# Optimization experiments

Hardware: AMD Instinct MI355X
Metric: run time of the kernel (lower is better)

The kernel has to match this reference:

```python
import jax, jax.numpy as jnp
import numpy as np

INF = 1000000000000.0
B, H, EMB = 64, 512, 512
V = 32000
S_ENC, S_SEQ = 512, 512
ENC2 = 512  # 2 * encoder_hidden_dim
NUM_OOV = 50


def setup_inputs() -> dict:
    key = jax.random.key(0)
    ks = jax.random.split(key, 24)
    s = 0.02
    nrm = lambda k, shp: jax.random.normal(k, shp, jnp.float32) * s
    inp = {}
    inp["input_ids"] = jax.random.randint(ks[0], (B,), 0, V)
    inp["prev_context"] = jax.random.normal(ks[1], (B, H), jnp.float32)
    inp["h0"] = jax.random.normal(ks[2], (1, B, H), jnp.float32)
    inp["c0"] = jax.random.normal(ks[3], (1, B, H), jnp.float32)
    inp["encoder_outputs"] = jax.random.normal(ks[4], (B, S_ENC, H), jnp.float32)
    inp["seqs_encoding"] = jax.random.normal(ks[5], (B, S_SEQ, ENC2), jnp.float32)
    inp["seqs_encoding_mask"] = jax.random.randint(ks[6], (B, S_SEQ), 0, 2).astype(bool)
    ext = jax.random.randint(ks[7], (B, S_SEQ), 0, V + NUM_OOV)
    inp["ext_idx"] = ext.at[0, 0].set(V + NUM_OOV - 1)  # pin max so num_oov=NUM_OOV
    # parameters (torch Linear convention: y = x @ W.T + b)
    inp["embed"] = nrm(ks[8], (V, EMB))
    inp["W_reduce"] = nrm(ks[9], (EMB, EMB + H)); inp["b_reduce"] = jnp.zeros((EMB,), jnp.float32)
    inp["W_key"] = nrm(ks[10], (H, H)); inp["b_key"] = jnp.zeros((H,), jnp.float32)
    inp["W_comb"] = nrm(ks[11], (H, 2 * H)); inp["b_comb"] = jnp.zeros((H,), jnp.float32)
    inp["W_seqkey"] = nrm(ks[12], (H, ENC2))
    inp["W_ih"] = nrm(ks[13], (4 * H, EMB)); inp["W_hh"] = nrm(ks[14], (4 * H, H))
    inp["b_ih"] = jnp.zeros((4 * H,), jnp.float32); inp["b_hh"] = jnp.zeros((4 * H,), jnp.float32)
    inp["W_out"] = nrm(ks[15], (V, H)); inp["b_out"] = jnp.zeros((V,), jnp.float32)
    return inp


def reference(input_ids, prev_context, h0, c0, encoder_outputs, seqs_encoding,
              seqs_encoding_mask, ext_idx, embed, W_reduce, b_reduce, W_key, b_key,
              W_comb, b_comb, W_seqkey, W_ih, W_hh, b_ih, b_hh, W_out, b_out):
    # embed + (dropout is identity at p=0 / eval) + reduce
    embedded = embed[input_ids]                                   # [B, EMB]
    x = jnp.concatenate([embedded, prev_context], axis=1) @ W_reduce.T + b_reduce  # [B, EMB]
    # single-step, single-layer LSTM (PyTorch gate order i, f, g, o)
    h, c = h0[0], c0[0]
    gates = x @ W_ih.T + b_ih + h @ W_hh.T + b_hh                 # [B, 4H]
    i, f, g, o = jnp.split(gates, 4, axis=-1)
    c1 = jax.nn.sigmoid(f) * c + jax.nn.sigmoid(i) * jnp.tanh(g)
    h1 = jax.nn.sigmoid(o) * jnp.tanh(c1)                         # [B, H]
    output = h1
    # masked attention over encoder_outputs
    enc_mask = encoder_outputs.sum(axis=-1) == 0                  # [B, S_enc]
    keys = encoder_outputs @ W_key.T + b_key                      # [B, S_enc, H]
    energies = jnp.einsum('bsh,bh->bs', keys, output)
    energies = jnp.where(enc_mask, 1e-12, energies)
    attn_weights = jax.nn.softmax(energies, axis=-1)
    context = jnp.einsum('bs,bsh->bh', attn_weights, encoder_outputs)  # [B, H]
    combined = jnp.tanh(jnp.concatenate([output, context], axis=1) @ W_comb.T + b_comb)
    logits = combined @ W_out.T + b_out                           # [B, V]
    # masked attention energies over token sequence for the copy mechanism
    seq_keys = jnp.tanh(seqs_encoding @ W_seqkey.T)               # [B, S_seq, H]
    seq_energies = jnp.einsum('bsh,bh->bs', seq_keys, output)
    seq_energies = jnp.where(seqs_encoding_mask, 1e-12, seq_energies)
    # extended vocab + scatter_max pointer-copy
    extended = jnp.concatenate([logits, jnp.zeros((B, NUM_OOV), logits.dtype)], axis=1)  # [B, V+OOV]
    copy = jnp.full_like(extended, -INF)
    copy = copy.at[jnp.arange(B)[:, None], ext_idx].max(seq_energies)
    copy = jnp.where(copy == -INF, 0.0, copy)
    out = extended + copy
    out = jnp.where(out == 0.0, -INF, out)
    out = jax.nn.log_softmax(out, axis=1)
    return (out, context, h1[None], c1[None], attn_weights)
```

## Files before the change

### kernel.cpp

```cpp
#include <hip/hip_runtime.h>
#include <math.h>

#define B_N    64
#define H_N    512
#define V_N    32000
#define S_N    512
#define VEXT   32050
#define INF_F  1000000000000.0f

typedef __attribute__((ext_vector_type(4))) float floatx4;
typedef __attribute__((ext_vector_type(8))) __bf16 bf16x8;

#define OFF_OUT0 0
#define OFF_CTX  (B_N * VEXT)
#define OFF_H1   (OFF_CTX + B_N * H_N)
#define OFF_C1   (OFF_H1 + B_N * H_N)
#define OFF_ATTN (OFF_C1 + B_N * H_N)

#define WS_FLAG   0
#define WS_X      16
#define WS_GATES  (WS_X + B_N * H_N)
#define WS_Q      (WS_GATES + B_N * 4 * H_N)
#define WS_KB     (WS_Q + B_N * H_N)
#define WS_EN     (WS_KB + B_N)
#define WS_COMB   (WS_EN + B_N * S_N)
#define WS_SEQE   (WS_COMB + B_N * H_N)
#define WS_WSKBF  (WS_SEQE + B_N * S_N)
#define WS_LOGITS (WS_WSKBF + (H_N * H_N) / 2)
#define WS_COPY   (WS_LOGITS + B_N * V_N)
#define WS_RMAX   (WS_COPY + B_N * VEXT)
#define WS_RSUM   (WS_RMAX + B_N)

__device__ __forceinline__ float sigm(float x) { return 1.0f / (1.0f + expf(-x)); }

__device__ __forceinline__ unsigned short f2bf(float f) {
    unsigned u = __float_as_uint(f);
    u += 0x7fffu + ((u >> 16) & 1u);
    return (unsigned short)(u >> 16);
}
__device__ __forceinline__ float bf2f(unsigned short h) {
    return __uint_as_float(((unsigned)h) << 16);
}

__device__ __forceinline__ unsigned enc_f(float f) {
    unsigned u = __float_as_uint(f);
    return (u & 0x80000000u) ? ~u : (u | 0x80000000u);
}
__device__ __forceinline__ float dec_f(unsigned e) {
    unsigned u = (e & 0x80000000u) ? (e & 0x7fffffffu) : ~e;
    return __uint_as_float(u);
}

__global__ __launch_bounds__(256) void kPre(
        const unsigned int* __restrict__ m, int* __restrict__ flag,
        const float* __restrict__ W, unsigned short* __restrict__ swzh,
        unsigned short* __restrict__ swzl, unsigned int* __restrict__ copyenc,
        unsigned int* __restrict__ rmax, float* __restrict__ rsum,
        float* __restrict__ ctx) {
    const int bx = blockIdx.x, tid = threadIdx.x;
    if (bx == 0) {
        __shared__ int any;
        if (tid == 0) any = 0;
        __syncthreads();
        int loc = 0;
        for (int i = tid; i < 8192; i += 256) loc |= (m[i] > 1u) ? 1 : 0;
        if (loc) any = 1;
        __syncthreads();
        if (tid == 0) *flag = any;
    } else if (bx < 129) {
        const int g = (bx - 1) * 256 + tid;
        const int t = g >> 10, kc = (g >> 6) & 15, lane = g & 63;
        const int r = t * 16 + (lane & 15);
        const int k = kc * 32 + (lane >> 4) * 8;
        const float* src = W + (size_t)r * 512 + k;
        ushort4 h0, h1, l0, l1;
        const float4 v0 = *(const float4*)(src);
        const float4 v1 = *(const float4*)(src + 4);
        h0.x = f2bf(v0.x); l0.x = f2bf(v0.x - bf2f(h0.x));
        h0.y = f2bf(v0.y); l0.y = f2bf(v0.y - bf2f(h0.y));
        h0.z = f2bf(v0.z); l0.z = f2bf(v0.z - bf2f(h0.z));
        h0.w = f2bf(v0.w); l0.w = f2bf(v0.w - bf2f(h0.w));
        h1.x = f2bf(v1.x); l1.x = f2bf(v1.x - bf2f(h1.x));
        h1.y = f2bf(v1.y); l1.y = f2bf(v1.y - bf2f(h1.y));
        h1.z = f2bf(v1.z); l1.z = f2bf(v1.z - bf2f(h1.z));
        h1.w = f2bf(v1.w); l1.w = f2bf(v1.w - bf2f(h1.w));
        *(ushort4*)(swzh + (size_t)g * 8) = h0;
        *(ushort4*)(swzh + (size_t)g * 8 + 4) = h1;
        *(ushort4*)(swzl + (size_t)g * 8) = l0;
        *(ushort4*)(swzl + (size_t)g * 8 + 4) = l1;
    } else if (bx < 2133) {
        const int fb = bx - 129;
        const unsigned NE = enc_f(-INF_F);
        if (fb == 0 && tid < B_N) {
            rmax[tid] = 0u;
            rsum[tid] = 0.0f;
        }
        int i0 = (fb * 256 + tid) * 4;
#pragma unroll
        for (int k = 0; k < 4; k++) {
            int i = i0 + k;
            if (i < B_N * VEXT) copyenc[i] = NE;
        }
    } else {
        const int zb = bx - 2133;
        const float4 z4 = {0.f, 0.f, 0.f, 0.f};
        *(float4*)(ctx + (size_t)(zb * 256 + tid) * 4) = z4;
    }
}

__global__ __launch_bounds__(256) void kEmbedReduce(
        const int* __restrict__ ids, const float* __restrict__ embed,
        const float* __restrict__ pctx, const float* __restrict__ Wred,
        const float* __restrict__ bred, float* __restrict__ x) {
    __shared__ float xc[1024];
    const int tid = threadIdx.x;
    const int b = blockIdx.x >> 1, half = blockIdx.x & 1;
    const float* er = embed + (size_t)ids[b] * 512;
    xc[tid] = er[tid];               xc[tid + 256] = er[tid + 256];
    xc[512 + tid] = pctx[b * 512 + tid]; xc[512 + tid + 256] = pctx[b * 512 + tid + 256];
    __syncthreads();
    const int j = half * 256 + tid;
    const float4* w4 = (const float4*)(Wred + (size_t)j * 1024);
    const float4* x4 = (const float4*)xc;
    float acc = bred[j];
    for (int k = 0; k < 256; k++) {
        float4 w = w4[k], xv = x4[k];
        acc += w.x * xv.x + w.y * xv.y + w.z * xv.z + w.w * xv.w;
    }
    x[b * 512 + j] = acc;
}

__global__ __launch_bounds__(256) void kGates(
        const float* __restrict__ x, const float* __restrict__ h0,
        const float* __restrict__ Wih, const float* __restrict__ Whh,
        const float* __restrict__ bih, const float* __restrict__ bhh,
        float* __restrict__ gates) {
    __shared__ float xl[512], hl[512];
    const int tid = threadIdx.x;
    const int b = blockIdx.x >> 3, part = blockIdx.x & 7;
    xl[tid] = x[b * 512 + tid];  xl[tid + 256] = x[b * 512 + tid + 256];
    hl[tid] = h0[b * 512 + tid]; hl[tid + 256] = h0[b * 512 + tid + 256];
    __syncthreads();
    const int j = part * 256 + tid;
    const float4* wi4 = (const float4*)(Wih + (size_t)j * 512);
    const float4* wh4 = (const float4*)(Whh + (size_t)j * 512);
    const float4* x4 = (const float4*)xl;
    const float4* h4 = (const float4*)hl;
    float acc = bih[j] + bhh[j];
    for (int k = 0; k < 128; k++) {
        float4 w = wi4[k], xv = x4[k];
        acc += w.x * xv.x + w.y * xv.y + w.z * xv.z + w.w * xv.w;
    }
    for (int k = 0; k < 128; k++) {
        float4 w = wh4[k], hv = h4[k];
        acc += w.x * hv.x + w.y * hv.y + w.z * hv.z + w.w * hv.w;
    }
    gates[(size_t)b * 2048 + j] = acc;
}

__global__ __launch_bounds__(256) void kLstm(
        const float* __restrict__ gates, const float* __restrict__ c0,
        float* __restrict__ h1o, float* __restrict__ c1o) {
    const int idx = blockIdx.x * 256 + threadIdx.x;
    const int b = idx >> 9, j = idx & 511;
    const float gi = gates[(size_t)b * 2048 + j];
    const float gf = gates[(size_t)b * 2048 + 512 + j];
    const float gg = gates[(size_t)b * 2048 + 1024 + j];
    const float go = gates[(size_t)b * 2048 + 1536 + j];
    const float cp = c0[idx];
    const float c1 = sigm(gf) * cp + sigm(gi) * tanhf(gg);
    const float h1 = sigm(go) * tanhf(c1);
    h1o[idx] = h1;
    c1o[idx] = c1;
}

__global__ __launch_bounds__(256) void kQ(
        const float* __restrict__ h1, const float* __restrict__ Wkey,
        const float* __restrict__ bkey, float* __restrict__ q, float* __restrict__ kb) {
    __shared__ float hl[512];
    __shared__ float rd[256];
    const int tid = threadIdx.x;
    const int b = blockIdx.x >> 1, half = blockIdx.x & 1;
    hl[tid] = h1[b * 512 + tid]; hl[tid + 256] = h1[b * 512 + tid + 256];
    __syncthreads();
    const int k = half * 256 + tid;
    float acc = 0.f;
#pragma unroll 4
    for (int h = 0; h < 512; h++) acc += hl[h] * Wkey[(size_t)h * 512 + k];
    q[b * 512 + k] = acc;
    if (half == 0) {
        float p = bkey[tid] * hl[tid] + bkey[tid + 256] * hl[tid + 256];
        rd[tid] = p; __syncthreads();
        for (int st = 128; st > 0; st >>= 1) {
            if (tid < st) rd[tid] += rd[tid + st];
            __syncthreads();
        }
        if (tid == 0) kb[b] = rd[0];
    }
}

__global__ __launch_bounds__(256) void kEnergies(
        const float* __restrict__ enc, const float* __restrict__ q,
        const float* __restrict__ kb, float* __restrict__ energ) {
    __shared__ float ql[512];
    __shared__ float pe[256], ps[256];
    const int tid = threadIdx.x;
    const int b = blockIdx.x >> 2;
    const int sc = (blockIdx.x & 3) * 128;
    ql[tid] = q[b * 512 + tid]; ql[tid + 256] = q[b * 512 + tid + 256];
    __syncthreads();
    const int r = tid & 127, hi = tid >> 7;
    const float4* row4 = (const float4*)(enc + (size_t)(b * 512 + sc + r) * 512 + hi * 256);
    const float4* q4 = (const float4*)(ql + hi * 256);
    float e = 0.f, ssum = 0.f;
#pragma unroll 4
    for (int k = 0; k < 64; k++) {
        float4 ev = row4[k], qv = q4[k];
        e += ev.x * qv.x + ev.y * qv.y + ev.z * qv.z + ev.w * qv.w;
        ssum += ev.x + ev.y + ev.z + ev.w;
    }
    pe[tid] = e; ps[tid] = ssum;
    __syncthreads();
    if (tid < 128) {
        float ee = pe[tid] + pe[tid + 128] + kb[b];
        float sm = ps[tid] + ps[tid + 128];
        if (sm == 0.0f) ee = 1e-12f;
        energ[b * 512 + sc + tid] = ee;
    }
}

__global__ __launch_bounds__(256) void kSoftmax(
        const float* __restrict__ energ, float* __restrict__ attn) {
    __shared__ float el[512];
    __shared__ float rd[256];
    const int tid = threadIdx.x, b = blockIdx.x;
    el[tid] = energ[b * 512 + tid]; el[tid + 256] = energ[b * 512 + tid + 256];
    __syncthreads();
    rd[tid] = fmaxf(el[tid], el[tid + 256]); __syncthreads();
    for (int st = 128; st > 0; st >>= 1) {
        if (tid < st) rd[tid] = fmaxf(rd[tid], rd[tid + st]);
        __syncthreads();
    }
    const float m = rd[0]; __syncthreads();
    float v0 = expf(el[tid] - m), v1 = expf(el[tid + 256] - m);
    rd[tid] = v0 + v1; __syncthreads();
    for (int st = 128; st > 0; st >>= 1) {
        if (tid < st) rd[tid] += rd[tid + st];
        __syncthreads();
    }
    const float inv = 1.0f / rd[0];
    attn[b * 512 + tid] = v0 * inv;
    attn[b * 512 + tid + 256] = v1 * inv;
}

__global__ __launch_bounds__(256) void kContext(
        const float* __restrict__ enc, const float* __restrict__ attn,
        float* __restrict__ ctx) {
    __shared__ float al[64];
    const int tid = threadIdx.x;
    const int b = blockIdx.x >> 3, sc = (blockIdx.x & 7) * 64;
    if (tid < 64) al[tid] = attn[b * 512 + sc + tid];
    __syncthreads();
    float a0 = 0.f, a1 = 0.f;
    for (int s = 0; s < 64; s++) {
        const float* row = enc + (size_t)(b * 512 + sc + s) * 512;
        const float av = al[s];
        a0 += av * row[tid];
        a1 += av * row[tid + 256];
    }
    atomicAdd(&ctx[b * 512 + tid], a0);
    atomicAdd(&ctx[b * 512 + tid + 256], a1);
}

__global__ __launch_bounds__(256) void kCombined(
        const float* __restrict__ h1, const float* __restrict__ ctx,
        const float* __restrict__ Wcomb, const float* __restrict__ bcomb,
        float* __restrict__ comb) {
    __shared__ float hc[1024];
    const int tid = threadIdx.x;
    const int b = blockIdx.x >> 1, half = blockIdx.x & 1;
    hc[tid] = h1[b * 512 + tid];        hc[tid + 256] = h1[b * 512 + tid + 256];
    hc[512 + tid] = ctx[b * 512 + tid]; hc[512 + tid + 256] = ctx[b * 512 + tid + 256];
    __syncthreads();
    const int j = half * 256 + tid;
    const float4* w4 = (const float4*)(Wcomb + (size_t)j * 1024);
    const float4* x4 = (const float4*)hc;
    float acc = bcomb[j];
    for (int k = 0; k < 256; k++) {
        float4 w = w4[k], xv = x4[k];
        acc += w.x * xv.x + w.y * xv.y + w.z * xv.z + w.w * xv.w;
    }
    comb[b * 512 + j] = tanhf(acc);
}

__global__ __launch_bounds__(256) void kLogits(
        const float* __restrict__ comb, const float* __restrict__ Wout,
        const float* __restrict__ bout, float* __restrict__ logits) {
    __shared__ float cl[4][32][64];
    const int tid = threadIdx.x;
    const int vt = tid & 63, kq = tid >> 6;
    const int v = blockIdx.x * 64 + vt;
    float acc[64];
#pragma unroll
    for (int i = 0; i < 64; i++) acc[i] = 0.f;
    for (int kc = 0; kc < 4; kc++) {
        __syncthreads();
        {
            const float4* s4 = (const float4*)(comb + (size_t)vt * 512 + kq * 128 + kc * 32);
#pragma unroll
            for (int qq = 0; qq < 8; qq++) {
                float4 vv = s4[qq];
                cl[kq][qq * 4 + 0][vt] = vv.x; cl[kq][qq * 4 + 1][vt] = vv.y;
                cl[kq][qq * 4 + 2][vt] = vv.z; cl[kq][qq * 4 + 3][vt] = vv.w;
            }
        }
        __syncthreads();
        float wreg[32];
        const float4* w4 = (const float4*)(Wout + (size_t)v * 512 + kq * 128 + kc * 32);
#pragma unroll
        for (int qq = 0; qq < 8; qq++) {
            float4 wv = w4[qq];
            wreg[qq * 4 + 0] = wv.x; wreg[qq * 4 + 1] = wv.y;
            wreg[qq * 4 + 2] = wv.z; wreg[qq * 4 + 3] = wv.w;
        }
#pragma unroll
        for (int kk = 0; kk < 32; kk++) {
            const float wv = wreg[kk];
            const float4* cp = (const float4*)&cl[kq][kk][0];
#pragma unroll
            for (int b4 = 0; b4 < 16; b4++) {
                float4 c4 = cp[b4];
                acc[b4 * 4 + 0] += wv * c4.x; acc[b4 * 4 + 1] += wv * c4.y;
                acc[b4 * 4 + 2] += wv * c4.z; acc[b4 * 4 + 3] += wv * c4.w;
            }
        }
    }
    float* red = &cl[0][0][0];
    __syncthreads();
    if (kq >= 2) {
#pragma unroll
        for (int b = 0; b < 64; b++) red[(kq - 2) * 4096 + vt * 64 + b] = acc[b];
    }
    __syncthreads();
    if (kq < 2) {
#pragma unroll
        for (int b = 0; b < 64; b++) acc[b] += red[kq * 4096 + vt * 64 + b];
    }
    __syncthreads();
    if (kq == 1) {
#pragma unroll
        for (int b = 0; b < 64; b++) red[vt * 64 + b] = acc[b];
    }
    __syncthreads();
    if (kq == 0) {
        const float bo = bout[v];
#pragma unroll
        for (int b = 0; b < 64; b++)
            logits[(size_t)b * 32000 + v] = acc[b] + red[vt * 64 + b] + bo;
    }
}

#define ACH 136
__global__ __launch_bounds__(512, 2) void kSeqGemm(
        const float* __restrict__ seqs, const unsigned short* __restrict__ swzh,
        const unsigned short* __restrict__ swzl, const float* __restrict__ h1g,
        const void* __restrict__ mask, const int* __restrict__ extix,
        const int* __restrict__ flag, unsigned int* __restrict__ copyenc) {
    __shared__ unsigned short a_hi[128 * ACH];
    __shared__ unsigned short a_lo[128 * ACH];
    __shared__ float h1l[512];
    __shared__ float partf[8][128];
    const int tid = threadIdx.x;
    const int m0 = blockIdx.x * 128;
    const int b = blockIdx.x >> 2;
    const int w = tid >> 6;
    const int lane = tid & 63;
    const int quad = lane >> 4;
    const int c16 = lane & 15;

    h1l[tid] = h1g[b * 512 + tid];

    floatx4 acc[8][4];
    const floatx4 zf = {0.f, 0.f, 0.f, 0.f};
#pragma unroll
    for (int i = 0; i < 8; i++)
#pragma unroll
        for (int j = 0; j < 4; j++) acc[i][j] = zf;

    const size_t boff = (size_t)(w * 64) * 512 + (size_t)lane * 8;
    const unsigned short* bh = swzh + boff;
    const unsigned short* bl = swzl + boff;

    const int srow = tid >> 2, sq = tid & 3;

    for (int c = 0; c < 4; c++) {
        __syncthreads();
        {
            const float* src = seqs + (size_t)(m0 + srow) * 512 + c * 128 + sq * 32;
            unsigned short* dh = &a_hi[srow * ACH + sq * 32];
            unsigned short* dl = &a_lo[srow * ACH + sq * 32];
#pragma unroll
            for (int i = 0; i < 8; i++) {
                float4 v = *(const float4*)(src + i * 4);
                ushort4 hv, lv;
                hv.x = f2bf(v.x); lv.x = f2bf(v.x - bf2f(hv.x));
                hv.y = f2bf(v.y); lv.y = f2bf(v.y - bf2f(hv.y));
                hv.z = f2bf(v.z); lv.z = f2bf(v.z - bf2f(hv.z));
                hv.w = f2bf(v.w); lv.w = f2bf(v.w - bf2f(hv.w));
                *(ushort4*)(dh + i * 4) = hv;
                *(ushort4*)(dl + i * 4) = lv;
            }
        }
        __syncthreads();
#pragma unroll
        for (int kcl = 0; kcl < 4; kcl++) {
            const int kc = c * 4 + kcl;
            bf16x8 bhf[4], blf[4];
#pragma unroll
            for (int nt = 0; nt < 4; nt++) {
                bhf[nt] = *(const bf16x8*)(bh + (size_t)(nt * 16 + kc) * 512);
                blf[nt] = *(const bf16x8*)(bl + (size_t)(nt * 16 + kc) * 512);
            }
#pragma unroll
            for (int ms = 0; ms < 8; ms++) {
                bf16x8 ah = *(const bf16x8*)&a_hi[(ms * 16 + c16) * ACH + kcl * 32 + quad * 8];
                bf16x8 al = *(const bf16x8*)&a_lo[(ms * 16 + c16) * ACH + kcl * 32 + quad * 8];
#pragma unroll
                for (int nt = 0; nt < 4; nt++) {
                    acc[ms][nt] = __builtin_amdgcn_mfma_f32_16x16x32_bf16(
                        ah, bhf[nt], acc[ms][nt], 0, 0, 0);
                    acc[ms][nt] = __builtin_amdgcn_mfma_f32_16x16x32_bf16(
                        al, bhf[nt], acc[ms][nt], 0, 0, 0);
                    acc[ms][nt] = __builtin_amdgcn_mfma_f32_16x16x32_bf16(
                        ah, blf[nt], acc[ms][nt], 0, 0, 0);
                }
            }
        }
    }

    float psum[32];
#pragma unroll
    for (int i = 0; i < 32; i++) psum[i] = 0.f;
#pragma unroll
    for (int ms = 0; ms < 8; ms++)
#pragma unroll
        for (int nt = 0; nt < 4; nt++) {
            const float hv = h1l[w * 64 + nt * 16 + c16];
#pragma unroll
            for (int r = 0; r < 4; r++)
                psum[ms * 4 + r] += tanhf(acc[ms][nt][r]) * hv;
        }
#pragma unroll
    for (int d = 1; d < 16; d <<= 1)
#pragma unroll
        for (int i = 0; i < 32; i++) psum[i] += __shfl_xor(psum[i], d);
    if (c16 == 0) {
#pragma unroll
        for (int ms = 0; ms < 8; ms++)
#pragma unroll
            for (int r = 0; r < 4; r++)
                partf[w][ms * 16 + quad * 4 + r] = psum[ms * 4 + r];
    }
    __syncthreads();
    if (tid < 128) {
        float s = 0.f;
#pragma unroll
        for (int ww = 0; ww < 8; ww++) s += partf[ww][tid];
        const int m = m0 + tid;
        bool mk;
        if (*flag) mk = ((const unsigned char*)mask)[m] != 0;
        else       mk = ((const int*)mask)[m] != 0;
        if (mk) s = 1e-12f;
        const int idx = extix[m];
        atomicMax(&copyenc[(size_t)b * VEXT + idx], enc_f(s));
    }
}

__global__ __launch_bounds__(256) void kFinal1(
        const float* __restrict__ logits, const unsigned int* __restrict__ copyenc,
        float* __restrict__ out0, unsigned int* __restrict__ rmax) {
    __shared__ float rd[4];
    const int tid = threadIdx.x;
    const int b = blockIdx.x >> 4, chunk = blockIdx.x & 15;
    const int base = chunk * 2048 + tid;
    const float* lrow = logits + (size_t)b * 32000;
    const unsigned int* crow = copyenc + (size_t)b * VEXT;
    float* orow = out0 + (size_t)b * VEXT;
    float lm = -3.0e38f;
#pragma unroll
    for (int k = 0; k < 8; k++) {
        const int j = base + k * 256;
        if (j < VEXT) {
            float ext = (j < 32000) ? lrow[j] : 0.0f;
            float cv = dec_f(crow[j]);
            if (cv == -INF_F) cv = 0.0f;
            float o = ext + cv;
            if (o == 0.0f) o = -INF_F;
            orow[j] = o;
            lm = fmaxf(lm, o);
        }
    }
#pragma unroll
    for (int d = 1; d < 64; d <<= 1) lm = fmaxf(lm, __shfl_xor(lm, d));
    if ((tid & 63) == 0) rd[tid >> 6] = lm;
    __syncthreads();
    if (tid == 0) {
        float m = fmaxf(fmaxf(rd[0], rd[1]), fmaxf(rd[2], rd[3]));
        atomicMax(&rmax[b], enc_f(m));
    }
}

__global__ __launch_bounds__(256) void kFinal2(
        const float* __restrict__ out0, const unsigned int* __restrict__ rmax,
        float* __restrict__ rsum) {
    __shared__ float rd[4];
    const int tid = threadIdx.x;
    const int b = blockIdx.x >> 4, chunk = blockIdx.x & 15;
    const int base = chunk * 2048 + tid;
    const float* orow = out0 + (size_t)b * VEXT;
    const float m = dec_f(rmax[b]);
    float s = 0.f;
#pragma unroll
    for (int k = 0; k < 8; k++) {
        const int j = base + k * 256;
        if (j < VEXT) s += expf(orow[j] - m);
    }
#pragma unroll
    for (int d = 1; d < 64; d <<= 1) s += __shfl_xor(s, d);
    if ((tid & 63) == 0) rd[tid >> 6] = s;
    __syncthreads();
    if (tid == 0) atomicAdd(&rsum[b], rd[0] + rd[1] + rd[2] + rd[3]);
}

__global__ __launch_bounds__(256) void kFinal3(
        float* __restrict__ out0, const unsigned int* __restrict__ rmax,
        const float* __restrict__ rsum) {
    const int tid = threadIdx.x;
    const int b = blockIdx.x >> 4, chunk = blockIdx.x & 15;
    const int base = chunk * 2048 + tid;
    float* orow = out0 + (size_t)b * VEXT;
    const float lse = dec_f(rmax[b]) + logf(rsum[b]);
#pragma unroll
    for (int k = 0; k < 8; k++) {
        const int j = base + k * 256;
        if (j < VEXT) orow[j] -= lse;
    }
}

extern "C" void kernel_launch(void* const* d_in, const int* in_sizes, int n_in,
                              void* d_out, int out_size, void* d_ws, size_t ws_size,
                              hipStream_t stream) {
    const int*   ids   = (const int*)d_in[0];
    const float* pctx  = (const float*)d_in[1];
    const float* h0    = (const float*)d_in[2];
    const float* c0    = (const float*)d_in[3];
    const float* enc   = (const float*)d_in[4];
    const float* seqs  = (const float*)d_in[5];
    const void*  mask  = d_in[6];
    const int*   extix = (const int*)d_in[7];
    const float* embed = (const float*)d_in[8];
    const float* Wred  = (const float*)d_in[9];
    const float* bred  = (const float*)d_in[10];
    const float* Wkey  = (const float*)d_in[11];
    const float* bkey  = (const float*)d_in[12];
    const float* Wcomb = (const float*)d_in[13];
    const float* bcomb = (const float*)d_in[14];
    const float* Wseqk = (const float*)d_in[15];
    const float* Wih   = (const float*)d_in[16];
    const float* Whh   = (const float*)d_in[17];
    const float* bih   = (const float*)d_in[18];
    const float* bhh   = (const float*)d_in[19];
    const float* Wout  = (const float*)d_in[20];
    const float* bout  = (const float*)d_in[21];
    (void)in_sizes; (void)n_in; (void)out_size; (void)ws_size;

    float* out = (float*)d_out;
    float* ws = (float*)d_ws;
    int* flag = (int*)ws;
    float* xws = ws + WS_X;
    float* gatesws = ws + WS_GATES;
    float* qws = ws + WS_Q;
    float* kbws = ws + WS_KB;
    float* enws = ws + WS_EN;
    float* combws = ws + WS_COMB;
    unsigned short* wskh = (unsigned short*)(ws + WS_WSKBF);
    float* logitsws = ws + WS_LOGITS;
    unsigned short* wskl = (unsigned short*)(ws + WS_LOGITS);
    unsigned int* copyenc = (unsigned int*)(ws + WS_COPY);
    unsigned int* rmax = (unsigned int*)(ws + WS_RMAX);
    float* rsum = ws + WS_RSUM;

    kPre<<<2165, 256, 0, stream>>>((const unsigned int*)mask, flag, Wseqk, wskh, wskl,
                                   copyenc, rmax, rsum, out + OFF_CTX);
    kEmbedReduce<<<128, 256, 0, stream>>>(ids, embed, pctx, Wred, bred, xws);
    kGates<<<512, 256, 0, stream>>>(xws, h0, Wih, Whh, bih, bhh, gatesws);
    kLstm<<<128, 256, 0, stream>>>(gatesws, c0, out + OFF_H1, out + OFF_C1);
    kSeqGemm<<<256, 512, 0, stream>>>(seqs, wskh, wskl, out + OFF_H1,
                                      mask, extix, flag, copyenc);
    kQ<<<128, 256, 0, stream>>>(out + OFF_H1, Wkey, bkey, qws, kbws);
    kEnergies<<<256, 256, 0, stream>>>(enc, qws, kbws, enws);
    kSoftmax<<<64, 256, 0, stream>>>(enws, out + OFF_ATTN);
    kContext<<<512, 256, 0, stream>>>(enc, out + OFF_ATTN, out + OFF_CTX);
    kCombined<<<128, 256, 0, stream>>>(out + OFF_H1, out + OFF_CTX, Wcomb, bcomb, combws);
    kLogits<<<500, 256, 0, stream>>>(combws, Wout, bout, logitsws);
    kFinal1<<<1024, 256, 0, stream>>>(logitsws, copyenc, out + OFF_OUT0, rmax);
    kFinal2<<<1024, 256, 0, stream>>>(out + OFF_OUT0, rmax, rsum);
    kFinal3<<<1024, 256, 0, stream>>>(out + OFF_OUT0, rmax, rsum);
}
```

Baseline: 591.6 us.

## Fuse three log-softmax passes into one register-resident kernel; halve seq GEMM tile

Replaces the three final kernels (max, sum-exp, normalize), which used global atomics and re-read the output, with one kernel per batch row of 1024 threads. Each thread keeps its 32 values in registers and does both reductions through shared memory. This removes two launches and two extra passes over the 64x32050 output. Separately, the sequence-key GEMM tile shrinks from 128 to 64 rows, doubling its grid to 512 blocks for better CU coverage, at the cost of reloading the B fragments more often. The fused kernel runs only 64 blocks, so the final stage may be limited by per-block bandwidth.

```diff
diff --git a/kernel.cpp b/kernel.cpp
--- a/kernel.cpp
+++ b/kernel.cpp
@@ -366,13 +366,13 @@
         const unsigned short* __restrict__ swzl, const float* __restrict__ h1g,
         const void* __restrict__ mask, const int* __restrict__ extix,
         const int* __restrict__ flag, unsigned int* __restrict__ copyenc) {
-    __shared__ unsigned short a_hi[128 * ACH];
-    __shared__ unsigned short a_lo[128 * ACH];
+    __shared__ unsigned short a_hi[64 * ACH];
+    __shared__ unsigned short a_lo[64 * ACH];
     __shared__ float h1l[512];
-    __shared__ float partf[8][128];
-    const int tid = threadIdx.x;
-    const int m0 = blockIdx.x * 128;
-    const int b = blockIdx.x >> 2;
+    __shared__ float partf[8][64];
+    const int tid = threadIdx.x;
+    const int m0 = blockIdx.x * 64;
+    const int b = blockIdx.x >> 3;
     const int w = tid >> 6;
     const int lane = tid & 63;
     const int quad = lane >> 4;
@@ -380,10 +380,10 @@
 
     h1l[tid] = h1g[b * 512 + tid];
 
-    floatx4 acc[8][4];
+    floatx4 acc[4][4];
     const floatx4 zf = {0.f, 0.f, 0.f, 0.f};
 #pragma unroll
-    for (int i = 0; i < 8; i++)
+    for (int i = 0; i < 4; i++)
 #pragma unroll
         for (int j = 0; j < 4; j++) acc[i][j] = zf;
 
@@ -391,16 +391,16 @@
     const unsigned short* bh = swzh + boff;
     const unsigned short* bl = swzl + boff;
 
-    const int srow = tid >> 2, sq = tid & 3;
+    const int srow = tid >> 3, sq = tid & 7;
 
     for (int c = 0; c < 4; c++) {
         __syncthreads();
         {
-            const float* src = seqs + (size_t)(m0 + srow) * 512 + c * 128 + sq * 32;
-            unsigned short* dh = &a_hi[srow * ACH + sq * 32];
-            unsigned short* dl = &a_lo[srow * ACH + sq * 32];
-#pragma unroll
-            for (int i = 0; i < 8; i++) {
+            const float* src = seqs + (size_t)(m0 + srow) * 512 + c * 128 + sq * 16;
+            unsigned short* dh = &a_hi[srow * ACH + sq * 16];
+            unsigned short* dl = &a_lo[srow * ACH + sq * 16];
+#pragma unroll
+            for (int i = 0; i < 4; i++) {
                 float4 v = *(const float4*)(src + i * 4);
                 ushort4 hv, lv;
                 hv.x = f2bf(v.x); lv.x = f2bf(v.x - bf2f(hv.x));
@@ -422,7 +422,7 @@
                 blf[nt] = *(const bf16x8*)(bl + (size_t)(nt * 16 + kc) * 512);
             }
 #pragma unroll
-            for (int ms = 0; ms < 8; ms++) {
+            for (int ms = 0; ms < 4; ms++) {
                 bf16x8 ah = *(const bf16x8*)&a_hi[(ms * 16 + c16) * ACH + kcl * 32 + quad * 8];
                 bf16x8 al = *(const bf16x8*)&a_lo[(ms * 16 + c16) * ACH + kcl * 32 + quad * 8];
 #pragma unroll
@@ -438,11 +438,11 @@
         }
     }
 
-    float psum[32];
-#pragma unroll
-    for (int i = 0; i < 32; i++) psum[i] = 0.f;
-#pragma unroll
-    for (int ms = 0; ms < 8; ms++)
+    float psum[16];
+#pragma unroll
+    for (int i = 0; i < 16; i++) psum[i] = 0.f;
+#pragma unroll
+    for (int ms = 0; ms < 4; ms++)
 #pragma unroll
         for (int nt = 0; nt < 4; nt++) {
             const float hv = h1l[w * 64 + nt * 16 + c16];
@@ -453,16 +453,16 @@
 #pragma unroll
     for (int d = 1; d < 16; d <<= 1)
 #pragma unroll
-        for (int i = 0; i < 32; i++) psum[i] += __shfl_xor(psum[i], d);
+        for (int i = 0; i < 16; i++) psum[i] += __shfl_xor(psum[i], d);
     if (c16 == 0) {
 #pragma unroll
-        for (int ms = 0; ms < 8; ms++)
+        for (int ms = 0; ms < 4; ms++)
 #pragma unroll
             for (int r = 0; r < 4; r++)
                 partf[w][ms * 16 + quad * 4 + r] = psum[ms * 4 + r];
     }
     __syncthreads();
-    if (tid < 128) {
+    if (tid < 64) {
         float s = 0.f;
 #pragma unroll
         for (int ww = 0; ww < 8; ww++) s += partf[ww][tid];
@@ -476,74 +476,54 @@
     }
 }
 
-__global__ __launch_bounds__(256) void kFinal1(
+__global__ __launch_bounds__(1024) void kFinal(
         const float* __restrict__ logits, const unsigned int* __restrict__ copyenc,
-        float* __restrict__ out0, unsigned int* __restrict__ rmax) {
-    __shared__ float rd[4];
-    const int tid = threadIdx.x;
-    const int b = blockIdx.x >> 4, chunk = blockIdx.x & 15;
-    const int base = chunk * 2048 + tid;
+        float* __restrict__ out0) {
+    __shared__ float redm[16];
+    __shared__ float reds[16];
+    const int b = blockIdx.x, tid = threadIdx.x;
     const float* lrow = logits + (size_t)b * 32000;
     const unsigned int* crow = copyenc + (size_t)b * VEXT;
     float* orow = out0 + (size_t)b * VEXT;
+    float o[32];
     float lm = -3.0e38f;
 #pragma unroll
-    for (int k = 0; k < 8; k++) {
-        const int j = base + k * 256;
+    for (int k = 0; k < 32; k++) {
+        const int j = k * 1024 + tid;
         if (j < VEXT) {
             float ext = (j < 32000) ? lrow[j] : 0.0f;
             float cv = dec_f(crow[j]);
             if (cv == -INF_F) cv = 0.0f;
-            float o = ext + cv;
-            if (o == 0.0f) o = -INF_F;
-            orow[j] = o;
-            lm = fmaxf(lm, o);
+            float v = ext + cv;
+            if (v == 0.0f) v = -INF_F;
+            o[k] = v;
+            lm = fmaxf(lm, v);
+        } else {
+            o[k] = -INF_F;
         }
     }
 #pragma unroll
     for (int d = 1; d < 64; d <<= 1) lm = fmaxf(lm, __shfl_xor(lm, d));
-    if ((tid & 63) == 0) rd[tid >> 6] = lm;
-    __syncthreads();
-    if (tid == 0) {
-        float m = fmaxf(fmaxf(rd[0], rd[1]), fmaxf(rd[2], rd[3]));
-        atomicMax(&rmax[b], enc_f(m));
-    }
-}
-
-__global__ __launch_bounds__(256) void kFinal2(
-        const float* __restrict__ out0, const unsigned int* __restrict__ rmax,
-        float* __restrict__ rsum) {
-    __shared__ float rd[4];
-    const int tid = threadIdx.x;
-    const int b = blockIdx.x >> 4, chunk = blockIdx.x & 15;
-    const int base = chunk * 2048 + tid;
-    const float* orow = out0 + (size_t)b * VEXT;
-    const float m = dec_f(rmax[b]);
+    if ((tid & 63) == 0) redm[tid >> 6] = lm;
+    __syncthreads();
+    float m = redm[0];
+#pragma unroll
+    for (int i = 1; i < 16; i++) m = fmaxf(m, redm[i]);
     float s = 0.f;
 #pragma unroll
-    for (int k = 0; k < 8; k++) {
-        const int j = base + k * 256;
-        if (j < VEXT) s += expf(orow[j] - m);
-    }
+    for (int k = 0; k < 32; k++) s += expf(o[k] - m);
 #pragma unroll
     for (int d = 1; d < 64; d <<= 1) s += __shfl_xor(s, d);
-    if ((tid & 63) == 0) rd[tid >> 6] = s;
-    __syncthreads();
-    if (tid == 0) atomicAdd(&rsum[b], rd[0] + rd[1] + rd[2] + rd[3]);
-}
-
-__global__ __launch_bounds__(256) void kFinal3(
-        float* __restrict__ out0, const unsigned int* __restrict__ rmax,
-        const float* __restrict__ rsum) {
-    const int tid = threadIdx.x;
-    const int b = blockIdx.x >> 4, chunk = blockIdx.x & 15;
-    const int base = chunk * 2048 + tid;
-    float* orow = out0 + (size_t)b * VEXT;
-    const float lse = dec_f(rmax[b]) + logf(rsum[b]);
-#pragma unroll
-    for (int k = 0; k < 8; k++) {
-        const int j = base + k * 256;
-        if (j < VEXT) orow[j] -= lse;
+    if ((tid & 63) == 0) reds[tid >> 6] = s;
+    __syncthreads();
+    float tot = reds[0];
+#pragma unroll
+    for (int i = 1; i < 16; i++) tot += reds[i];
+    const float lse = m + logf(tot);
+#pragma unroll
+    for (int k = 0; k < 32; k++) {
+        const int j = k * 1024 + tid;
+        if (j < VEXT) orow[j] = o[k] - lse;
     }
 }
 
@@ -595,7 +575,7 @@
     kEmbedReduce<<<128, 256, 0, stream>>>(ids, embed, pctx, Wred, bred, xws);
     kGates<<<512, 256, 0, stream>>>(xws, h0, Wih, Whh, bih, bhh, gatesws);
     kLstm<<<128, 256, 0, stream>>>(gatesws, c0, out + OFF_H1, out + OFF_C1);
-    kSeqGemm<<<256, 512, 0, stream>>>(seqs, wskh, wskl, out + OFF_H1,
+    kSeqGemm<<<512, 512, 0, stream>>>(seqs, wskh, wskl, out + OFF_H1,
                                       mask, extix, flag, copyenc);
     kQ<<<128, 256, 0, stream>>>(out + OFF_H1, Wkey, bkey, qws, kbws);
     kEnergies<<<256, 256, 0, stream>>>(enc, qws, kbws, enws);
@@ -603,7 +583,5 @@
     kContext<<<512, 256, 0, stream>>>(enc, out + OFF_ATTN, out + OFF_CTX);
     kCombined<<<128, 256, 0, stream>>>(out + OFF_H1, out + OFF_CTX, Wcomb, bcomb, combws);
     kLogits<<<500, 256, 0, stream>>>(combws, Wout, bout, logitsws);
-    kFinal1<<<1024, 256, 0, stream>>>(logitsws, copyenc, out + OFF_OUT0, rmax);
-    kFinal2<<<1024, 256, 0, stream>>>(out + OFF_OUT0, rmax, rsum);
-    kFinal3<<<1024, 256, 0, stream>>>(out + OFF_OUT0, rmax, rsum);
-}
+    kFinal<<<64, 1024, 0, stream>>>(logitsws, copyenc, out + OFF_OUT0);
+}
```

Measured after the change: 572.9 us. 1.03x faster.
